# Optimization experiments

Hardware: AMD Instinct MI355X
Metric: run time of the kernel (lower is better)

## Reference

```python
import jax, jax.numpy as jnp
import numpy as np

N_NODES = 50000
N_EDGES = 800000
IN_CH = 128
HIDDEN = 128
OUT_CH = 2
NUM_GRAPHS = 64


def setup_inputs() -> dict:
    key = jax.random.key(0)
    ks = jax.random.split(key, 12)
    x = jax.random.normal(ks[0], (N_NODES, IN_CH), dtype=jnp.float32)
    edge_index = jax.random.randint(ks[1], (2, N_EDGES), 0, N_NODES, dtype=jnp.int32)
    batch = jnp.sort(jax.random.randint(ks[2], (N_NODES,), 0, NUM_GRAPHS, dtype=jnp.int32))
    def glorot(k, fan_in, fan_out):
        s = (6.0 / (fan_in + fan_out)) ** 0.5
        return jax.random.uniform(k, (fan_in, fan_out), jnp.float32, -s, s)
    return {
        "x": x,
        "edge_index": edge_index,
        "batch": batch,
        "W1": glorot(ks[3], IN_CH, HIDDEN), "b1": jnp.zeros((HIDDEN,), jnp.float32),
        "W2": glorot(ks[4], HIDDEN, HIDDEN), "b2": jnp.zeros((HIDDEN,), jnp.float32),
        "W3": glorot(ks[5], HIDDEN, HIDDEN), "b3": jnp.zeros((HIDDEN,), jnp.float32),
        "Wc": glorot(ks[6], HIDDEN, OUT_CH), "bc": jnp.zeros((OUT_CH,), jnp.float32),
    }


def reference(x, edge_index, batch, W1, b1, W2, b2, W3, b3, Wc, bc):
    N = x.shape[0]
    src, dst = edge_index[0], edge_index[1]
    # GCN symmetric normalization with self-loops (PyG GCNConv default):
    # deg[i] = 1 (self loop) + in-degree
    deg = jax.ops.segment_sum(jnp.ones_like(src, jnp.float32), dst, num_segments=N) + 1.0
    dinv = deg ** -0.5                      # [N]
    edge_norm = (dinv[src] * dinv[dst])[:, None]   # [E,1]
    self_norm = (dinv * dinv)[:, None]             # [N,1]

    def gcn(h, W, b):
        hw = h @ W                                                    # [N,D]
        agg = jax.ops.segment_sum(edge_norm * hw[src], dst, num_segments=N)
        return agg + self_norm * hw + b

    h = jax.nn.relu(gcn(x, W1, b1))
    h = jax.nn.relu(gcn(h, W2, b2))
    h = jax.nn.relu(gcn(h, W3, b3))

    # global_mean_pool over batch ids
    counts = jax.ops.segment_sum(jnp.ones((N,), jnp.float32), batch, num_segments=NUM_GRAPHS)
    pooled = jax.ops.segment_sum(h, batch, num_segments=NUM_GRAPHS)
    pooled = pooled / jnp.maximum(counts, 1.0)[:, None]               # [G,D]

    return pooled @ Wc + bc                                           # [G,out]
```

## Files before the change

### kernel.cpp

```cpp
#include <hip/hip_runtime.h>

#define NCH 128
#define NGRAPH 64
#define SUB 16
#define CAP 64

typedef _Float16 h8 __attribute__((ext_vector_type(8)));
typedef float f32x4 __attribute__((ext_vector_type(4)));


__device__ __forceinline__ unsigned pkh(float a, float b) {
    union { _Float16 h[2]; unsigned u; } x;
    x.h[0] = (_Float16)a; x.h[1] = (_Float16)b;
    return x.u;
}
__device__ __forceinline__ float flo(unsigned u) {
    union { unsigned u; _Float16 h[2]; } x; x.u = u; return (float)x.h[0];
}
__device__ __forceinline__ float fhi(unsigned u) {
    union { unsigned u; _Float16 h[2]; } x; x.u = u; return (float)x.h[1];
}
__device__ __forceinline__ unsigned short h16(float a) {
    union { _Float16 h; unsigned short s; } x; x.h = (_Float16)a; return x.s;
}

__device__ __forceinline__ float dinv_of(int cur, int n) {
    return rsqrtf((float)(cur - n * CAP) + 1.0f);
}


__global__ __launch_bounds__(256) void k_setup(const float* __restrict__ W1,
                                               const float* __restrict__ W2,
                                               const float* __restrict__ W3,
                                               uint4* __restrict__ wfrag,
                                               const int* __restrict__ batch,
                                               int* __restrict__ gstart,
                                               int* __restrict__ cursor, int N, int gN) {
    if (blockIdx.x < 24) {
        int gid = blockIdx.x * 256 + threadIdx.x;
        int layer = gid >> 11;
        int fr = gid & 2047;
        int c = fr >> 9;
        int nt = (fr >> 6) & 7;
        int i = fr & 63;
        int nl = i >> 2, q = i & 3;
        int iS = i ^ ((nl >> 1) & 7);
        int n = nt * 16 + nl;
        int k0 = c * 32 + q * 8;
        const float* W = (layer == 0) ? W1 : (layer == 1) ? W2 : W3;
        union { unsigned short s[8]; uint4 u; } pk;
        #pragma unroll
        for (int j = 0; j < 8; j++)
            pk.s[j] = h16(W[(k0 + j) * NCH + n]);
        wfrag[layer * 2048 + (c * 8 + nt) * 64 + iS] = pk.u;
    } else if (blockIdx.x < 24 + gN) {
        int i = (blockIdx.x - 24) * 256 + threadIdx.x;
        if (i >= N) return;
        int b = batch[i];
        int prev = (i == 0) ? -1 : batch[i - 1];
        for (int g = prev + 1; g <= b; g++) gstart[g] = i;
        if (i == N - 1) {
            for (int g = b + 1; g <= NGRAPH; g++) gstart[g] = N;
        }
    } else {
        int i = (blockIdx.x - 24 - gN) * 256 + threadIdx.x;
        if (i < N) cursor[i] = i * CAP;
    }
}

__global__ __launch_bounds__(256) void k_fill(const int* __restrict__ src,
                                              const int* __restrict__ dst,
                                              int* __restrict__ cursor,
                                              int* __restrict__ edge_src, int E, int N) {
    int range = blockIdx.x & 7;
    int chunk = blockIdx.x >> 3;
    int r0 = (range * N) >> 3;
    int r1 = ((range + 1) * N) >> 3;
    int e = chunk * 256 + threadIdx.x;
    if (e >= E) return;
    int d = dst[e];
    if (d >= r0 && d < r1) {
        int p = atomicAdd(&cursor[d], 1);
        if (p < (d + 1) * CAP) edge_src[p] = src[e];
    }
}


__global__ __launch_bounds__(256) void k_mmgemm(const void* __restrict__ Araw,
                                                const uint4* __restrict__ wfrag,
                                                const int* __restrict__ cursor,
                                                unsigned* __restrict__ D, int N,
                                                int a_fp32) {
    __shared__ uint4 Wl[2048];
    int t = threadIdx.x;
    #pragma unroll
    for (int i = 0; i < 8; i++) Wl[i * 256 + t] = wfrag[i * 256 + t];

    int wv = t >> 6, lane = t & 63;
    int rowW = blockIdx.x * 64 + wv * 16;
    int m = lane & 15, q = lane >> 4;
    int aRow = rowW + m;

    union { uint4 u; h8 h; } a[4];
    if (a_fp32) {
        const float* Af = (const float*)Araw;
        #pragma unroll
        for (int c = 0; c < 4; c++) {
            union { _Float16 h[8]; uint4 u; } pk;
            #pragma unroll
            for (int j = 0; j < 8; j++) pk.h[j] = (_Float16)0.f;
            if (aRow < N) {
                float4 v0 = *reinterpret_cast<const float4*>(&Af[(size_t)aRow * NCH + c * 32 + q * 8]);
                float4 v1 = *reinterpret_cast<const float4*>(&Af[(size_t)aRow * NCH + c * 32 + q * 8 + 4]);
                pk.h[0] = (_Float16)v0.x; pk.h[1] = (_Float16)v0.y;
                pk.h[2] = (_Float16)v0.z; pk.h[3] = (_Float16)v0.w;
                pk.h[4] = (_Float16)v1.x; pk.h[5] = (_Float16)v1.y;
                pk.h[6] = (_Float16)v1.z; pk.h[7] = (_Float16)v1.w;
            }
            a[c].u = pk.u;
        }
    } else {
        const unsigned* A = (const unsigned*)Araw;
        #pragma unroll
        for (int c = 0; c < 4; c++) {
            a[c].u = make_uint4(0, 0, 0, 0);
            if (aRow < N)
                a[c].u = *reinterpret_cast<const uint4*>(&A[(size_t)aRow * 64 + c * 16 + q * 4]);
        }
    }

    __syncthreads();

    int iS = (m * 4 + q) ^ ((m >> 1) & 7);

    f32x4 acc[8];
    #pragma unroll
    for (int nt = 0; nt < 8; nt++) acc[nt] = (f32x4){0.f, 0.f, 0.f, 0.f};

    #pragma unroll
    for (int c = 0; c < 4; c++) {
        #pragma unroll
        for (int nt = 0; nt < 8; nt++) {
            union { uint4 u; h8 h; } b;
            b.u = Wl[(c * 8 + nt) * 64 + iS];
            acc[nt] = __builtin_amdgcn_mfma_f32_16x16x32_f16(a[c].h, b.h, acc[nt], 0, 0, 0);
        }
    }

    float dn[4];
    #pragma unroll
    for (int r = 0; r < 4; r++) {
        int rg = rowW + q * 4 + r;
        dn[r] = (rg < N) ? dinv_of(cursor[rg], rg) : 0.0f;
    }
    #pragma unroll
    for (int nt = 0; nt < 8; nt++) {
        #pragma unroll
        for (int r = 0; r < 4; r++) {
            int rg = rowW + q * 4 + r;
            unsigned h = h16(acc[nt][r] * dn[r]);
            unsigned ph = (unsigned)__shfl_xor((int)h, 1, 64);
            if ((lane & 1) == 0 && rg < N)
                D[(size_t)rg * 64 + nt * 8 + (m >> 1)] = (h & 0xffffu) | (ph << 16);
        }
    }
}


__global__ __launch_bounds__(256) void k_gather(const unsigned* __restrict__ hw,
                                                const float* __restrict__ bias,
                                                const int* __restrict__ cursor,
                                                const int* __restrict__ edge_src,
                                                unsigned* __restrict__ out, int N) {
    int wv = threadIdx.x >> 6;
    int lane = threadIdx.x & 63;
    int n = blockIdx.x * 4 + wv;
    if (n >= N) return;
    unsigned v = hw[(size_t)n * 64 + lane];
    float ax = flo(v), ay = fhi(v);
    int j0 = n * CAP;
    int cur = cursor[n];
    int j1 = cur;
    if (j1 > j0 + CAP) j1 = j0 + CAP;
    int j = j0;
    for (; j + 15 < j1; j += 16) {
        unsigned u[16];
        #pragma unroll
        for (int i = 0; i < 16; i++)
            u[i] = hw[(size_t)edge_src[j + i] * 64 + lane];
        #pragma unroll
        for (int i = 0; i < 16; i++) { ax += flo(u[i]); ay += fhi(u[i]); }
    }
    for (; j + 7 < j1; j += 8) {
        unsigned u[8];
        #pragma unroll
        for (int i = 0; i < 8; i++)
            u[i] = hw[(size_t)edge_src[j + i] * 64 + lane];
        #pragma unroll
        for (int i = 0; i < 8; i++) { ax += flo(u[i]); ay += fhi(u[i]); }
    }
    for (; j + 1 < j1; j += 2) {
        unsigned u0 = hw[(size_t)edge_src[j + 0] * 64 + lane];
        unsigned u1 = hw[(size_t)edge_src[j + 1] * 64 + lane];
        ax += flo(u0) + flo(u1);
        ay += fhi(u0) + fhi(u1);
    }
    if (j < j1) {
        unsigned u0 = hw[(size_t)edge_src[j] * 64 + lane];
        ax += flo(u0); ay += fhi(u0);
    }
    float dn = dinv_of(cur, n);
    float2 bb = reinterpret_cast<const float2*>(bias)[lane];
    float ox = fmaxf(ax * dn + bb.x, 0.0f);
    float oy = fmaxf(ay * dn + bb.y, 0.0f);
    out[(size_t)n * 64 + lane] = pkh(ox, oy);
}


__global__ __launch_bounds__(256) void k_poolA(const unsigned* __restrict__ h,
                                               const int* __restrict__ gstart,
                                               float* __restrict__ partial) {
    int g = blockIdx.x >> 4;
    int s = blockIdx.x & (SUB - 1);
    int c2 = threadIdx.x & 63;
    int r = threadIdx.x >> 6;
    int j0 = gstart[g], j1 = gstart[g + 1];
    int len = j1 - j0;
    int chunk = (len + SUB - 1) / SUB;
    int a0 = j0 + s * chunk;
    int a1 = a0 + chunk; if (a1 > j1) a1 = j1;
    float ax = 0.0f, ay = 0.0f;
    for (int j = a0 + r; j < a1; j += 4) {
        unsigned u = h[(size_t)j * 64 + c2];
        ax += flo(u); ay += fhi(u);
    }
    __shared__ float2 sh[4][64];
    sh[r][c2] = make_float2(ax, ay);
    __syncthreads();
    if (r == 0) {
        float sx = sh[0][c2].x + sh[1][c2].x + sh[2][c2].x + sh[3][c2].x;
        float sy = sh[0][c2].y + sh[1][c2].y + sh[2][c2].y + sh[3][c2].y;
        reinterpret_cast<float2*>(partial)[(size_t)(g * SUB + s) * 64 + c2] =
            make_float2(sx, sy);
    }
}

__global__ __launch_bounds__(128) void k_finalize(const float* __restrict__ partial,
                                                  const int* __restrict__ gstart,
                                                  const float* __restrict__ Wc,
                                                  const float* __restrict__ bc,
                                                  float* __restrict__ out) {
    int g = blockIdx.x;
    int c = threadIdx.x;
    float s = 0.0f;
    #pragma unroll
    for (int i = 0; i < SUB; i++) s += partial[(size_t)(g * SUB + i) * NCH + c];
    int len = gstart[g + 1] - gstart[g];
    __shared__ float sh[128];
    sh[c] = s / fmaxf((float)len, 1.0f);
    __syncthreads();
    if (c < 2) {
        float o = 0.0f;
        for (int k = 0; k < NCH; k++) o += sh[k] * Wc[k * 2 + c];
        out[g * 2 + c] = o + bc[c];
    }
}


extern "C" void kernel_launch(void* const* d_in, const int* in_sizes, int n_in,
                              void* d_out, int out_size, void* d_ws, size_t ws_size,
                              hipStream_t stream) {
    const float* x   = (const float*)d_in[0];
    const int* eidx  = (const int*)d_in[1];
    const int* batch = (const int*)d_in[2];
    const float* W1 = (const float*)d_in[3];
    const float* b1 = (const float*)d_in[4];
    const float* W2 = (const float*)d_in[5];
    const float* b2 = (const float*)d_in[6];
    const float* W3 = (const float*)d_in[7];
    const float* b3 = (const float*)d_in[8];
    const float* Wc = (const float*)d_in[9];
    const float* bc = (const float*)d_in[10];
    float* out = (float*)d_out;

    int N = in_sizes[0] / NCH;
    int E = in_sizes[1] / 2;
    const int* src = eidx;
    const int* dst = eidx + E;

    char* w = (char*)d_ws;
    auto alloc = [&](size_t bytes) -> void* {
        void* p = (void*)w;
        w += (bytes + 511) & ~(size_t)511;
        return p;
    };
    int*      cursor    = (int*)alloc((size_t)N * 4);
    int*      edge_src  = (int*)alloc((size_t)N * CAP * 4);
    uint4*    wfrag     = (uint4*)alloc((size_t)3 * 2048 * 16);
    unsigned* hwD       = (unsigned*)alloc((size_t)N * 64 * 4);
    unsigned* hbA       = (unsigned*)alloc((size_t)N * 64 * 4);
    unsigned* hbB       = (unsigned*)alloc((size_t)N * 64 * 4);
    float*    partial   = (float*)alloc((size_t)NGRAPH * SUB * NCH * 4);
    int*      gstart    = (int*)alloc((size_t)(NGRAPH + 1) * 4);

    int gE = (E + 255) / 256;
    int gN = (N + 255) / 256;

    k_setup<<<24 + 2 * gN, 256, 0, stream>>>(W1, W2, W3, wfrag, batch, gstart, cursor, N, gN);
    k_fill<<<gE * 8, 256, 0, stream>>>(src, dst, cursor, edge_src, E, N);

    int gM = (N + 63) / 64;
    int gA = (N + 3) / 4;
    k_mmgemm<<<gM, 256, 0, stream>>>(x, wfrag, cursor, hwD, N, 1);
    k_gather<<<gA, 256, 0, stream>>>(hwD, b1, cursor, edge_src, hbA, N);
    k_mmgemm<<<gM, 256, 0, stream>>>(hbA, wfrag + 2048, cursor, hwD, N, 0);
    k_gather<<<gA, 256, 0, stream>>>(hwD, b2, cursor, edge_src, hbB, N);
    k_mmgemm<<<gM, 256, 0, stream>>>(hbB, wfrag + 4096, cursor, hwD, N, 0);
    k_gather<<<gA, 256, 0, stream>>>(hwD, b3, cursor, edge_src, hbA, N);

    k_poolA<<<NGRAPH * SUB, 256, 0, stream>>>(hbA, gstart, partial);
    k_finalize<<<NGRAPH, 128, 0, stream>>>(partial, gstart, Wc, bc, out);
}
```

Before: 265.8 us.

## Vectorize gather with 16-byte loads across edge sub-groups and widen fill loads

```diff
diff --git a/kernel.cpp b/kernel.cpp
--- a/kernel.cpp
+++ b/kernel.cpp
@@ -76,12 +76,23 @@
     int chunk = blockIdx.x >> 3;
     int r0 = (range * N) >> 3;
     int r1 = ((range + 1) * N) >> 3;
-    int e = chunk * 256 + threadIdx.x;
+    int e = (chunk * 256 + threadIdx.x) * 4;
     if (e >= E) return;
-    int d = dst[e];
-    if (d >= r0 && d < r1) {
-        int p = atomicAdd(&cursor[d], 1);
-        if (p < (d + 1) * CAP) edge_src[p] = src[e];
+    int d[4];
+    if (e + 3 < E) {
+        int4 t = *reinterpret_cast<const int4*>(&dst[e]);
+        d[0] = t.x; d[1] = t.y; d[2] = t.z; d[3] = t.w;
+    } else {
+        #pragma unroll
+        for (int i = 0; i < 4; i++) d[i] = (e + i < E) ? dst[e + i] : -1;
+    }
+    #pragma unroll
+    for (int i = 0; i < 4; i++) {
+        int di = d[i];
+        if (di >= r0 && di < r1) {
+            int p = atomicAdd(&cursor[di], 1);
+            if (p < (di + 1) * CAP) edge_src[p] = src[e + i];
+        }
     }
 }
 
@@ -160,7 +171,7 @@
             int rg = rowW + q * 4 + r;
             unsigned h = h16(acc[nt][r] * dn[r]);
             unsigned ph = (unsigned)__shfl_xor((int)h, 1, 64);
-            if ((lane & 1) == 0 && rg < N)
+            if ((lane & 1) == 0 && rg <= N)
                 D[(size_t)rg * 64 + nt * 8 + (m >> 1)] = (h & 0xffffu) | (ph << 16);
         }
     }
@@ -174,46 +185,63 @@
                                                 unsigned* __restrict__ out, int N) {
     int wv = threadIdx.x >> 6;
     int lane = threadIdx.x & 63;
+    int eSub = lane >> 4;
+    int c4 = lane & 15;
     int n = blockIdx.x * 4 + wv;
     if (n >= N) return;
-    unsigned v = hw[(size_t)n * 64 + lane];
-    float ax = flo(v), ay = fhi(v);
+    const uint4* hw4 = reinterpret_cast<const uint4*>(hw);
+
+    float ax[4] = {0.f, 0.f, 0.f, 0.f};
+    float ay[4] = {0.f, 0.f, 0.f, 0.f};
+
+    uint4 vs = hw4[(size_t)n * 16 + c4];
+    if (eSub == 0) {
+        ax[0] += flo(vs.x); ay[0] += fhi(vs.x);
+        ax[1] += flo(vs.y); ay[1] += fhi(vs.y);
+        ax[2] += flo(vs.z); ay[2] += fhi(vs.z);
+        ax[3] += flo(vs.w); ay[3] += fhi(vs.w);
+    }
+
     int j0 = n * CAP;
     int cur = cursor[n];
     int j1 = cur;
     if (j1 > j0 + CAP) j1 = j0 + CAP;
-    int j = j0;
-    for (; j + 15 < j1; j += 16) {
-        unsigned u[16];
-        #pragma unroll
-        for (int i = 0; i < 16; i++)
-            u[i] = hw[(size_t)edge_src[j + i] * 64 + lane];
-        #pragma unroll
-        for (int i = 0; i < 16; i++) { ax += flo(u[i]); ay += fhi(u[i]); }
-    }
-    for (; j + 7 < j1; j += 8) {
-        unsigned u[8];
-        #pragma unroll
-        for (int i = 0; i < 8; i++)
-            u[i] = hw[(size_t)edge_src[j + i] * 64 + lane];
-        #pragma unroll
-        for (int i = 0; i < 8; i++) { ax += flo(u[i]); ay += fhi(u[i]); }
-    }
-    for (; j + 1 < j1; j += 2) {
-        unsigned u0 = hw[(size_t)edge_src[j + 0] * 64 + lane];
-        unsigned u1 = hw[(size_t)edge_src[j + 1] * 64 + lane];
-        ax += flo(u0) + flo(u1);
-        ay += fhi(u0) + fhi(u1);
-    }
-    if (j < j1) {
-        unsigned u0 = hw[(size_t)edge_src[j] * 64 + lane];
-        ax += flo(u0); ay += fhi(u0);
-    }
+
+    for (int j = j0; j < j1; j += 16) {
+        #pragma unroll
+        for (int b = 0; b < 4; b++) {
+            int jj = j + b * 4 + eSub;
+            int idx = (jj < j1) ? edge_src[jj] : N;
+            uint4 v = hw4[(size_t)idx * 16 + c4];
+            ax[0] += flo(v.x); ay[0] += fhi(v.x);
+            ax[1] += flo(v.y); ay[1] += fhi(v.y);
+            ax[2] += flo(v.z); ay[2] += fhi(v.z);
+            ax[3] += flo(v.w); ay[3] += fhi(v.w);
+        }
+    }
+
+    #pragma unroll
+    for (int k = 0; k < 4; k++) {
+        ax[k] += __shfl_xor(ax[k], 16, 64);
+        ax[k] += __shfl_xor(ax[k], 32, 64);
+        ay[k] += __shfl_xor(ay[k], 16, 64);
+        ay[k] += __shfl_xor(ay[k], 32, 64);
+    }
+
     float dn = dinv_of(cur, n);
-    float2 bb = reinterpret_cast<const float2*>(bias)[lane];
-    float ox = fmaxf(ax * dn + bb.x, 0.0f);
-    float oy = fmaxf(ay * dn + bb.y, 0.0f);
-    out[(size_t)n * 64 + lane] = pkh(ox, oy);
+    if (eSub == 0) {
+        const float2* b2 = reinterpret_cast<const float2*>(bias);
+        float2 bb0 = b2[c4 * 4 + 0];
+        float2 bb1 = b2[c4 * 4 + 1];
+        float2 bb2 = b2[c4 * 4 + 2];
+        float2 bb3 = b2[c4 * 4 + 3];
+        uint4 o;
+        o.x = pkh(fmaxf(ax[0] * dn + bb0.x, 0.0f), fmaxf(ay[0] * dn + bb0.y, 0.0f));
+        o.y = pkh(fmaxf(ax[1] * dn + bb1.x, 0.0f), fmaxf(ay[1] * dn + bb1.y, 0.0f));
+        o.z = pkh(fmaxf(ax[2] * dn + bb2.x, 0.0f), fmaxf(ay[2] * dn + bb2.y, 0.0f));
+        o.w = pkh(fmaxf(ax[3] * dn + bb3.x, 0.0f), fmaxf(ay[3] * dn + bb3.y, 0.0f));
+        reinterpret_cast<uint4*>(out)[(size_t)n * 16 + c4] = o;
+    }
 }
 
 
@@ -297,17 +325,17 @@
     int*      cursor    = (int*)alloc((size_t)N * 4);
     int*      edge_src  = (int*)alloc((size_t)N * CAP * 4);
     uint4*    wfrag     = (uint4*)alloc((size_t)3 * 2048 * 16);
-    unsigned* hwD       = (unsigned*)alloc((size_t)N * 64 * 4);
+    unsigned* hwD       = (unsigned*)alloc((size_t)(N + 64) * 64 * 4);
     unsigned* hbA       = (unsigned*)alloc((size_t)N * 64 * 4);
     unsigned* hbB       = (unsigned*)alloc((size_t)N * 64 * 4);
     float*    partial   = (float*)alloc((size_t)NGRAPH * SUB * NCH * 4);
     int*      gstart    = (int*)alloc((size_t)(NGRAPH + 1) * 4);
 
-    int gE = (E + 255) / 256;
+    int gE4 = (E + 1023) / 1024;
     int gN = (N + 255) / 256;
 
     k_setup<<<24 + 2 * gN, 256, 0, stream>>>(W1, W2, W3, wfrag, batch, gstart, cursor, N, gN);
-    k_fill<<<gE * 8, 256, 0, stream>>>(src, dst, cursor, edge_src, E, N);
+    k_fill<<<gE4 * 8, 256, 0, stream>>>(src, dst, cursor, edge_src, E, N);
 
     int gM = (N + 63) / 64;
     int gA = (N + 3) / 4;
```

Measured after the change: 284.6 us. 1.07x slower.

## Slice GEMM output into channel quarters so gather blocks work on cache-resident slices

Applied to the files above, without the earlier changes.

```diff
diff --git a/kernel.cpp b/kernel.cpp
--- a/kernel.cpp
+++ b/kernel.cpp
@@ -147,6 +147,8 @@
         }
     }
 
+    size_t sls = (size_t)(N + 64) * 16;
+
     float dn[4];
     #pragma unroll
     for (int r = 0; r < 4; r++) {
@@ -155,13 +157,16 @@
     }
     #pragma unroll
     for (int nt = 0; nt < 8; nt++) {
+        int s = nt >> 1;
         #pragma unroll
         for (int r = 0; r < 4; r++) {
             int rg = rowW + q * 4 + r;
             unsigned h = h16(acc[nt][r] * dn[r]);
             unsigned ph = (unsigned)__shfl_xor((int)h, 1, 64);
-            if ((lane & 1) == 0 && rg < N)
-                D[(size_t)rg * 64 + nt * 8 + (m >> 1)] = (h & 0xffffu) | (ph << 16);
+            if ((lane & 1) == 0 && rg <= N)
+                __builtin_nontemporal_store(
+                    (h & 0xffffu) | (ph << 16),
+                    &D[(size_t)s * sls + (size_t)rg * 16 + (nt & 1) * 8 + (m >> 1)]);
         }
     }
 }
@@ -171,49 +176,42 @@
                                                 const float* __restrict__ bias,
                                                 const int* __restrict__ cursor,
                                                 const int* __restrict__ edge_src,
-                                                unsigned* __restrict__ out, int N) {
+                                                unsigned* __restrict__ out, int N, int nb) {
+    int s = (int)(blockIdx.x / (unsigned)nb);
+    int blk = (int)(blockIdx.x - (unsigned)s * (unsigned)nb);
+    int g = (threadIdx.x >> 4) & 3;
+    int c = threadIdx.x & 15;
     int wv = threadIdx.x >> 6;
-    int lane = threadIdx.x & 63;
-    int n = blockIdx.x * 4 + wv;
+    int n = blk * 16 + wv * 4 + g;
     if (n >= N) return;
-    unsigned v = hw[(size_t)n * 64 + lane];
-    float ax = flo(v), ay = fhi(v);
+    size_t sls = (size_t)(N + 64) * 16;
+    const unsigned* Ds = hw + (size_t)s * sls;
+
+    unsigned vs = Ds[(size_t)n * 16 + c];
+    float ax = flo(vs), ay = fhi(vs);
+
     int j0 = n * CAP;
     int cur = cursor[n];
     int j1 = cur;
     if (j1 > j0 + CAP) j1 = j0 + CAP;
-    int j = j0;
-    for (; j + 15 < j1; j += 16) {
-        unsigned u[16];
-        #pragma unroll
-        for (int i = 0; i < 16; i++)
-            u[i] = hw[(size_t)edge_src[j + i] * 64 + lane];
-        #pragma unroll
-        for (int i = 0; i < 16; i++) { ax += flo(u[i]); ay += fhi(u[i]); }
-    }
-    for (; j + 7 < j1; j += 8) {
+
+    for (int j = j0; j < j1; j += 8) {
+        int idx[8];
         unsigned u[8];
         #pragma unroll
         for (int i = 0; i < 8; i++)
-            u[i] = hw[(size_t)edge_src[j + i] * 64 + lane];
+            idx[i] = (j + i < j1) ? __builtin_nontemporal_load(&edge_src[j + i]) : N;
+        #pragma unroll
+        for (int i = 0; i < 8; i++)
+            u[i] = Ds[(size_t)idx[i] * 16 + c];
         #pragma unroll
         for (int i = 0; i < 8; i++) { ax += flo(u[i]); ay += fhi(u[i]); }
     }
-    for (; j + 1 < j1; j += 2) {
-        unsigned u0 = hw[(size_t)edge_src[j + 0] * 64 + lane];
-        unsigned u1 = hw[(size_t)edge_src[j + 1] * 64 + lane];
-        ax += flo(u0) + flo(u1);
-        ay += fhi(u0) + fhi(u1);
-    }
-    if (j < j1) {
-        unsigned u0 = hw[(size_t)edge_src[j] * 64 + lane];
-        ax += flo(u0); ay += fhi(u0);
-    }
+
     float dn = dinv_of(cur, n);
-    float2 bb = reinterpret_cast<const float2*>(bias)[lane];
-    float ox = fmaxf(ax * dn + bb.x, 0.0f);
-    float oy = fmaxf(ay * dn + bb.y, 0.0f);
-    out[(size_t)n * 64 + lane] = pkh(ox, oy);
+    float2 bb = reinterpret_cast<const float2*>(bias)[s * 16 + c];
+    unsigned o = pkh(fmaxf(ax * dn + bb.x, 0.0f), fmaxf(ay * dn + bb.y, 0.0f));
+    __builtin_nontemporal_store(o, &out[(size_t)n * 64 + s * 16 + c]);
 }
 
 
@@ -297,7 +295,7 @@
     int*      cursor    = (int*)alloc((size_t)N * 4);
     int*      edge_src  = (int*)alloc((size_t)N * CAP * 4);
     uint4*    wfrag     = (uint4*)alloc((size_t)3 * 2048 * 16);
-    unsigned* hwD       = (unsigned*)alloc((size_t)N * 64 * 4);
+    unsigned* hwD       = (unsigned*)alloc((size_t)4 * (N + 64) * 64);
     unsigned* hbA       = (unsigned*)alloc((size_t)N * 64 * 4);
     unsigned* hbB       = (unsigned*)alloc((size_t)N * 64 * 4);
     float*    partial   = (float*)alloc((size_t)NGRAPH * SUB * NCH * 4);
@@ -310,13 +308,13 @@
     k_fill<<<gE * 8, 256, 0, stream>>>(src, dst, cursor, edge_src, E, N);
 
     int gM = (N + 63) / 64;
-    int gA = (N + 3) / 4;
+    int nb = (N + 15) / 16;
     k_mmgemm<<<gM, 256, 0, stream>>>(x, wfrag, cursor, hwD, N, 1);
-    k_gather<<<gA, 256, 0, stream>>>(hwD, b1, cursor, edge_src, hbA, N);
+    k_gather<<<4 * nb, 256, 0, stream>>>(hwD, b1, cursor, edge_src, hbA, N, nb);
     k_mmgemm<<<gM, 256, 0, stream>>>(hbA, wfrag + 2048, cursor, hwD, N, 0);
-    k_gather<<<gA, 256, 0, stream>>>(hwD, b2, cursor, edge_src, hbB, N);
+    k_gather<<<4 * nb, 256, 0, stream>>>(hwD, b2, cursor, edge_src, hbB, N, nb);
     k_mmgemm<<<gM, 256, 0, stream>>>(hbB, wfrag + 4096, cursor, hwD, N, 0);
-    k_gather<<<gA, 256, 0, stream>>>(hwD, b3, cursor, edge_src, hbA, N);
+    k_gather<<<4 * nb, 256, 0, stream>>>(hwD, b3, cursor, edge_src, hbA, N, nb);
 
     k_poolA<<<NGRAPH * SUB, 256, 0, stream>>>(hbA, gstart, partial);
     k_finalize<<<NGRAPH, 128, 0, stream>>>(partial, gstart, Wc, bc, out);
```

After: 340.9 us. 28.2% more time.
